# Kernel optimization log

Hardware: AMD Instinct MI355X
Metric: run time of the kernel (lower is better)

The kernel has to match this reference:

```python
import jax, jax.numpy as jnp
import numpy as np

E = 800000
NUM_RADIAL = 6
HIDDEN = 128
OUT = 128
NUM_NODES = 50000


def setup_inputs() -> dict:
    key = jax.random.key(0)
    ks = jax.random.split(key, 12)
    x = jax.random.normal(ks[0], (E, HIDDEN), dtype=jnp.float32)
    rbf = jax.random.uniform(ks[1], (E, NUM_RADIAL), dtype=jnp.float32)
    i = jax.random.randint(ks[2], (E,), 0, NUM_NODES, dtype=jnp.int64)
    s = 1.0 / np.sqrt(HIDDEN)
    W_rbf = jax.random.normal(ks[3], (HIDDEN, NUM_RADIAL), dtype=jnp.float32) / np.sqrt(NUM_RADIAL)
    W1 = jax.random.normal(ks[4], (HIDDEN, HIDDEN), dtype=jnp.float32) * s
    b1 = jnp.zeros((HIDDEN,), dtype=jnp.float32)
    W2 = jax.random.normal(ks[5], (HIDDEN, HIDDEN), dtype=jnp.float32) * s
    b2 = jnp.zeros((HIDDEN,), dtype=jnp.float32)
    W3 = jax.random.normal(ks[6], (HIDDEN, HIDDEN), dtype=jnp.float32) * s
    b3 = jnp.zeros((HIDDEN,), dtype=jnp.float32)
    W_out = jax.random.normal(ks[7], (OUT, HIDDEN), dtype=jnp.float32) * s
    return {"x": x, "rbf": rbf, "i": i, "num_nodes": NUM_NODES,
            "W_rbf": W_rbf, "W1": W1, "b1": b1, "W2": W2, "b2": b2,
            "W3": W3, "b3": b3, "W_out": W_out}


def reference(x, rbf, i, num_nodes, W_rbf, W1, b1, W2, b2, W3, b3, W_out):
    # edge-wise: lin_rbf(rbf) * x, then scatter-add to nodes
    m = (rbf @ W_rbf.T) * x                      # [E, H]
    h = jax.ops.segment_sum(m, i, num_segments=num_nodes)  # [N, H]
    # MLP stack with swish activation
    h = jax.nn.silu(h @ W1.T + b1)
    h = jax.nn.silu(h @ W2.T + b2)
    h = jax.nn.silu(h @ W3.T + b3)
    return h @ W_out.T                           # [N, OUT]
```

## Files before the change

### kernel.cpp

```cpp
#include <hip/hip_runtime.h>
#include <hip/hip_bf16.h>

#define H 128
#define NR 6
#define MT 128
#define HS 136

typedef __attribute__((ext_vector_type(8))) short short8_t;
typedef __attribute__((ext_vector_type(4))) float f32x4;

__device__ __forceinline__ float silu_f(float v) {
    return v / (1.0f + __expf(-v));
}

__device__ __forceinline__ unsigned short bf16_rne(float f) {
    unsigned u = __float_as_uint(f);
    u += 0x7FFF + ((u >> 16) & 1);
    return (unsigned short)(u >> 16);
}
__device__ __forceinline__ float bf16_to_f(unsigned short s) {
    return __uint_as_float(((unsigned)s) << 16);
}

__global__ __launch_bounds__(256) void hist_k(const int* __restrict__ idx,
                                              int* __restrict__ counts, int E) {
    int i = blockIdx.x * 256 + threadIdx.x;
    if (i < E) atomicAdd(&counts[idx[i]], 1);
}

__global__ __launch_bounds__(1024) void scan_k(const int* __restrict__ counts,
                                               int* __restrict__ offsets, int N) {
    __shared__ int wsum[16];
    __shared__ int runv;
    const int tid = threadIdx.x, lane = tid & 63, wv = tid >> 6;
    if (tid == 0) runv = 0;
    __syncthreads();
    for (int base = 0; base < N; base += 1024) {
        const int j = base + tid;
        const int v_in = (j < N) ? counts[j] : 0;
        int v = v_in;
        #pragma unroll
        for (int d = 1; d < 64; d <<= 1) {
            int u = __shfl_up(v, d);
            if (lane >= d) v += u;
        }
        if (lane == 63) wsum[wv] = v;
        __syncthreads();
        if (tid < 16) {
            int s = wsum[tid];
            #pragma unroll
            for (int d = 1; d < 16; d <<= 1) {
                int u = __shfl_up(s, d);
                if (tid >= d) s += u;
            }
            wsum[tid] = s;
        }
        __syncthreads();
        const int wexcl = (wv == 0) ? 0 : wsum[wv - 1];
        const int r0 = runv;
        if (j < N) offsets[j] = r0 + wexcl + (v - v_in);
        const int tot = wsum[15];
        __syncthreads();
        if (tid == 0) runv = r0 + tot;
        __syncthreads();
    }
    if (tid == 0) offsets[N] = runv;
}

__global__ __launch_bounds__(256) void fill_k(const int* __restrict__ idx,
                                              const int* __restrict__ offsets,
                                              int* __restrict__ cursor,
                                              int* __restrict__ elist, int E) {
    int i = blockIdx.x * 256 + threadIdx.x;
    if (i < E) {
        int node = idx[i];
        int pos = atomicAdd(&cursor[node], 1);
        elist[offsets[node] + pos] = i;
    }
}

__global__ __launch_bounds__(256) void gather_k(
    const float* __restrict__ x, const float* __restrict__ rbf,
    const float* __restrict__ W_rbf,
    const int* __restrict__ offsets, const int* __restrict__ elist,
    float* __restrict__ h, int N)
{
    const int t = threadIdx.x;
    const int lane = t & 63;
    const int node = blockIdx.x * 4 + (t >> 6);
    if (node >= N) return;

    const float4* wp = (const float4*)(W_rbf + lane * 12);
    const float4 wa = wp[0], wb = wp[1], wc = wp[2];
    const float wr0[NR] = {wa.x, wa.y, wa.z, wa.w, wb.x, wb.y};
    const float wr1[NR] = {wb.z, wb.w, wc.x, wc.y, wc.z, wc.w};

    const int beg = offsets[node], end = offsets[node + 1];
    float ax = 0.f, ay = 0.f;

    for (int base = beg; base < end; base += 64) {
        const int cnt = min(64, end - base);
        const int e_lane = (lane < cnt) ? elist[base + lane] : 0;
        int p = 0;
        for (; p + 4 <= cnt; p += 4) {
            int ev[4];
            float2 xv[4];
            float2 rv[4][3];
            #pragma unroll
            for (int q = 0; q < 4; ++q) ev[q] = __shfl(e_lane, p + q);
            #pragma unroll
            for (int q = 0; q < 4; ++q) {
                const size_t e = (size_t)ev[q];
                xv[q] = *(const float2*)(x + e * H + lane * 2);
                const float2* rp = (const float2*)(rbf + e * NR);
                rv[q][0] = rp[0]; rv[q][1] = rp[1]; rv[q][2] = rp[2];
            }
            #pragma unroll
            for (int q = 0; q < 4; ++q) {
                const float rr[NR] = {rv[q][0].x, rv[q][0].y, rv[q][1].x,
                                      rv[q][1].y, rv[q][2].x, rv[q][2].y};
                float m0 = 0.f, m1 = 0.f;
                #pragma unroll
                for (int j = 0; j < NR; ++j) { m0 += rr[j] * wr0[j]; m1 += rr[j] * wr1[j]; }
                ax += m0 * xv[q].x;
                ay += m1 * xv[q].y;
            }
        }
        for (; p < cnt; ++p) {
            const size_t e = (size_t)__shfl(e_lane, p);
            const float2 xv0 = *(const float2*)(x + e * H + lane * 2);
            const float2* rp = (const float2*)(rbf + e * NR);
            const float2 ra = rp[0], rb2 = rp[1], rc2 = rp[2];
            const float rr[NR] = {ra.x, ra.y, rb2.x, rb2.y, rc2.x, rc2.y};
            float m0 = 0.f, m1 = 0.f;
            #pragma unroll
            for (int j = 0; j < NR; ++j) { m0 += rr[j] * wr0[j]; m1 += rr[j] * wr1[j]; }
            ax += m0 * xv0.x;
            ay += m1 * xv0.y;
        }
    }
    *(float2*)(h + (size_t)node * H + lane * 2) = make_float2(ax, ay);
}


__device__ __forceinline__ void stage_w_lds(const float* __restrict__ Wg,
        unsigned short* w_hi, unsigned short* w_lo, int t)
{
    for (int i = t * 4; i < H * H; i += 2048) {
        const float4 v = *(const float4*)(Wg + i);
        const int c = i >> 7, k = i & 127;
        ushort4 hi4, lo4;
        hi4.x = bf16_rne(v.x); lo4.x = bf16_rne(v.x - bf16_to_f(hi4.x));
        hi4.y = bf16_rne(v.y); lo4.y = bf16_rne(v.y - bf16_to_f(hi4.y));
        hi4.z = bf16_rne(v.z); lo4.z = bf16_rne(v.z - bf16_to_f(hi4.z));
        hi4.w = bf16_rne(v.w); lo4.w = bf16_rne(v.w - bf16_to_f(hi4.w));
        *(ushort4*)&w_hi[c * HS + k] = hi4;
        *(ushort4*)&w_lo[c * HS + k] = lo4;
    }
}

__device__ __forceinline__ void compute_gemm(
    const unsigned short* h_hi, const unsigned short* h_lo,
    const unsigned short* w_hi, const unsigned short* w_lo,
    const float* bl, int wv, int lr, int quad, f32x4 (&acc)[8])
{
    short8_t a_hi[4], a_lo[4];
    const int row = wv * 16 + lr;
    #pragma unroll
    for (int kb = 0; kb < 4; ++kb) {
        const int off = row * HS + kb * 32 + quad * 8;
        a_hi[kb] = *(const short8_t*)&h_hi[off];
        a_lo[kb] = *(const short8_t*)&h_lo[off];
    }
    #pragma unroll
    for (int ct = 0; ct < 8; ct += 2) {
        const int c0 = ct * 16 + lr, c1 = (ct + 1) * 16 + lr;
        const float bb0 = bl[c0], bb1 = bl[c1];
        f32x4 A0 = {bb0, bb0, bb0, bb0}, A1 = {bb1, bb1, bb1, bb1};
        short8_t b0h[4], b0l[4], b1h[4], b1l[4];
        #pragma unroll
        for (int kb = 0; kb < 4; ++kb) {
            const int o0 = c0 * HS + kb * 32 + quad * 8;
            const int o1 = c1 * HS + kb * 32 + quad * 8;
            b0h[kb] = *(const short8_t*)&w_hi[o0];
            b0l[kb] = *(const short8_t*)&w_lo[o0];
            b1h[kb] = *(const short8_t*)&w_hi[o1];
            b1l[kb] = *(const short8_t*)&w_lo[o1];
        }
        #pragma unroll
        for (int kb = 0; kb < 4; ++kb) {
            A0 = __builtin_amdgcn_mfma_f32_16x16x32_bf16(a_hi[kb], b0h[kb], A0, 0, 0, 0);
            A1 = __builtin_amdgcn_mfma_f32_16x16x32_bf16(a_hi[kb], b1h[kb], A1, 0, 0, 0);
            A0 = __builtin_amdgcn_mfma_f32_16x16x32_bf16(a_hi[kb], b0l[kb], A0, 0, 0, 0);
            A1 = __builtin_amdgcn_mfma_f32_16x16x32_bf16(a_hi[kb], b1l[kb], A1, 0, 0, 0);
            A0 = __builtin_amdgcn_mfma_f32_16x16x32_bf16(a_lo[kb], b0h[kb], A0, 0, 0, 0);
            A1 = __builtin_amdgcn_mfma_f32_16x16x32_bf16(a_lo[kb], b1h[kb], A1, 0, 0, 0);
        }
        acc[ct] = A0;
        acc[ct + 1] = A1;
    }
}

__device__ __forceinline__ void epilogue_silu(
    unsigned short* h_hi, unsigned short* h_lo,
    f32x4 (&acc)[8], int wv, int lr, int quad)
{
    #pragma unroll
    for (int ct = 0; ct < 8; ++ct)
        #pragma unroll
        for (int r = 0; r < 4; ++r) {
            const int row = wv * 16 + quad * 4 + r;
            const int col = ct * 16 + lr;
            const float v = silu_f(acc[ct][r]);
            const unsigned short hi = bf16_rne(v);
            h_hi[row * HS + col] = hi;
            h_lo[row * HS + col] = bf16_rne(v - bf16_to_f(hi));
        }
}

__global__ __launch_bounds__(512, 2) void mlp_mfma(
    const float* __restrict__ hg,
    const float* __restrict__ W1, const float* __restrict__ b1,
    const float* __restrict__ W2, const float* __restrict__ b2,
    const float* __restrict__ W3, const float* __restrict__ b3,
    const float* __restrict__ Wo,
    float* __restrict__ out, int N)
{
    __shared__ unsigned short h_hi[H * HS], h_lo[H * HS];
    __shared__ unsigned short w_hi[H * HS], w_lo[H * HS];
    __shared__ float bl[H];

    const int t = threadIdx.x;
    const int lane = t & 63;
    const int wv = t >> 6;
    const int lr = lane & 15;
    const int quad = lane >> 4;
    const int row0 = blockIdx.x * MT;

    for (int i = t * 4; i < MT * H; i += 2048) {
        const int r = i >> 7, k = i & 127;
        const int row = row0 + r;
        const float4 v = (row < N) ? *(const float4*)(hg + (size_t)row * H + k)
                                   : make_float4(0.f, 0.f, 0.f, 0.f);
        ushort4 hi4, lo4;
        hi4.x = bf16_rne(v.x); lo4.x = bf16_rne(v.x - bf16_to_f(hi4.x));
        hi4.y = bf16_rne(v.y); lo4.y = bf16_rne(v.y - bf16_to_f(hi4.y));
        hi4.z = bf16_rne(v.z); lo4.z = bf16_rne(v.z - bf16_to_f(hi4.z));
        hi4.w = bf16_rne(v.w); lo4.w = bf16_rne(v.w - bf16_to_f(hi4.w));
        *(ushort4*)&h_hi[r * HS + k] = hi4;
        *(ushort4*)&h_lo[r * HS + k] = lo4;
    }
    stage_w_lds(W1, w_hi, w_lo, t);
    if (t < H) bl[t] = b1[t];
    __syncthreads();

    f32x4 acc[8];

    compute_gemm(h_hi, h_lo, w_hi, w_lo, bl, wv, lr, quad, acc);
    __syncthreads();
    epilogue_silu(h_hi, h_lo, acc, wv, lr, quad);
    stage_w_lds(W2, w_hi, w_lo, t);
    if (t < H) bl[t] = b2[t];
    __syncthreads();

    compute_gemm(h_hi, h_lo, w_hi, w_lo, bl, wv, lr, quad, acc);
    __syncthreads();
    epilogue_silu(h_hi, h_lo, acc, wv, lr, quad);
    stage_w_lds(W3, w_hi, w_lo, t);
    if (t < H) bl[t] = b3[t];
    __syncthreads();

    compute_gemm(h_hi, h_lo, w_hi, w_lo, bl, wv, lr, quad, acc);
    __syncthreads();
    epilogue_silu(h_hi, h_lo, acc, wv, lr, quad);
    stage_w_lds(Wo, w_hi, w_lo, t);
    if (t < H) bl[t] = 0.f;
    __syncthreads();

    compute_gemm(h_hi, h_lo, w_hi, w_lo, bl, wv, lr, quad, acc);

    #pragma unroll
    for (int ct = 0; ct < 8; ++ct)
        #pragma unroll
        for (int r = 0; r < 4; ++r) {
            const int row = row0 + wv * 16 + quad * 4 + r;
            if (row < N) out[(size_t)row * H + ct * 16 + lr] = acc[ct][r];
        }
}

static inline size_t align256(size_t v) { return (v + 255) & ~(size_t)255; }

extern "C" void kernel_launch(void* const* d_in, const int* in_sizes, int n_in,
                              void* d_out, int out_size, void* d_ws, size_t ws_size,
                              hipStream_t stream) {
    const float* x     = (const float*)d_in[0];
    const float* rbf   = (const float*)d_in[1];
    const int*   idx   = (const int*)d_in[2];
    const float* W_rbf = (const float*)d_in[4];
    const float* W1    = (const float*)d_in[5];
    const float* b1    = (const float*)d_in[6];
    const float* W2    = (const float*)d_in[7];
    const float* b2    = (const float*)d_in[8];
    const float* W3    = (const float*)d_in[9];
    const float* b3    = (const float*)d_in[10];
    const float* Wo    = (const float*)d_in[11];
    float* out = (float*)d_out;

    const int E = in_sizes[0] / H;
    const int N = out_size / H;

    char* ws = (char*)d_ws;
    size_t off = 0;
    float* h       = (float*)(ws + off); off = align256(off + (size_t)N * H * 4);
    int*   counts  = (int*)(ws + off);   off = align256(off + (size_t)N * 4);
    int*   cursor  = (int*)(ws + off);   off = align256(off + (size_t)N * 4);
    int*   offsets = (int*)(ws + off);   off = align256(off + (size_t)(N + 1) * 4);
    int*   elist   = (int*)(ws + off);   off = align256(off + (size_t)E * 4);

    hipMemsetAsync(counts, 0, (char*)offsets - (char*)counts, stream);

    hist_k<<<(E + 255) / 256, 256, 0, stream>>>(idx, counts, E);
    scan_k<<<1, 1024, 0, stream>>>(counts, offsets, N);
    fill_k<<<(E + 255) / 256, 256, 0, stream>>>(idx, offsets, cursor, elist, E);
    gather_k<<<(N + 3) / 4, 256, 0, stream>>>(x, rbf, W_rbf, offsets, elist, h, N);
    mlp_mfma<<<(N + MT - 1) / MT, 512, 0, stream>>>(h, W1, b1, W2, b2, W3, b3, Wo, out, N);
}
```

Before: 797.6 us.

## Fuse edge gather into MLP kernel and pre-split weights into bf16 hi/lo

Removes the separate gather kernel and its global h buffer. The gather now runs inside the MLP kernel and writes the bf16 hi/lo split straight into shared memory, with each wave handling 16 nodes and half-waves taking alternate edges using float4 loads. Weight hi/lo splitting moves to a small pre-kernel so each MLP block only copies ready-made bf16 data into shared memory. The cost is that the irregular gather now runs inside a large-LDS, low-occupancy block (only ~391 blocks), which can reduce the memory-level parallelism available for the random x reads.

```diff
diff --git a/kernel.cpp b/kernel.cpp
--- a/kernel.cpp
+++ b/kernel.cpp
@@ -1,5 +1,4 @@
 #include <hip/hip_runtime.h>
-#include <hip/hip_bf16.h>
 
 #define H 128
 #define NR 6
@@ -79,83 +78,38 @@
     }
 }
 
-__global__ __launch_bounds__(256) void gather_k(
-    const float* __restrict__ x, const float* __restrict__ rbf,
-    const float* __restrict__ W_rbf,
-    const int* __restrict__ offsets, const int* __restrict__ elist,
-    float* __restrict__ h, int N)
-{
-    const int t = threadIdx.x;
-    const int lane = t & 63;
-    const int node = blockIdx.x * 4 + (t >> 6);
-    if (node >= N) return;
-
-    const float4* wp = (const float4*)(W_rbf + lane * 12);
-    const float4 wa = wp[0], wb = wp[1], wc = wp[2];
-    const float wr0[NR] = {wa.x, wa.y, wa.z, wa.w, wb.x, wb.y};
-    const float wr1[NR] = {wb.z, wb.w, wc.x, wc.y, wc.z, wc.w};
-
-    const int beg = offsets[node], end = offsets[node + 1];
-    float ax = 0.f, ay = 0.f;
-
-    for (int base = beg; base < end; base += 64) {
-        const int cnt = min(64, end - base);
-        const int e_lane = (lane < cnt) ? elist[base + lane] : 0;
-        int p = 0;
-        for (; p + 4 <= cnt; p += 4) {
-            int ev[4];
-            float2 xv[4];
-            float2 rv[4][3];
-            #pragma unroll
-            for (int q = 0; q < 4; ++q) ev[q] = __shfl(e_lane, p + q);
-            #pragma unroll
-            for (int q = 0; q < 4; ++q) {
-                const size_t e = (size_t)ev[q];
-                xv[q] = *(const float2*)(x + e * H + lane * 2);
-                const float2* rp = (const float2*)(rbf + e * NR);
-                rv[q][0] = rp[0]; rv[q][1] = rp[1]; rv[q][2] = rp[2];
-            }
-            #pragma unroll
-            for (int q = 0; q < 4; ++q) {
-                const float rr[NR] = {rv[q][0].x, rv[q][0].y, rv[q][1].x,
-                                      rv[q][1].y, rv[q][2].x, rv[q][2].y};
-                float m0 = 0.f, m1 = 0.f;
-                #pragma unroll
-                for (int j = 0; j < NR; ++j) { m0 += rr[j] * wr0[j]; m1 += rr[j] * wr1[j]; }
-                ax += m0 * xv[q].x;
-                ay += m1 * xv[q].y;
-            }
-        }
-        for (; p < cnt; ++p) {
-            const size_t e = (size_t)__shfl(e_lane, p);
-            const float2 xv0 = *(const float2*)(x + e * H + lane * 2);
-            const float2* rp = (const float2*)(rbf + e * NR);
-            const float2 ra = rp[0], rb2 = rp[1], rc2 = rp[2];
-            const float rr[NR] = {ra.x, ra.y, rb2.x, rb2.y, rc2.x, rc2.y};
-            float m0 = 0.f, m1 = 0.f;
-            #pragma unroll
-            for (int j = 0; j < NR; ++j) { m0 += rr[j] * wr0[j]; m1 += rr[j] * wr1[j]; }
-            ax += m0 * xv0.x;
-            ay += m1 * xv0.y;
-        }
-    }
-    *(float2*)(h + (size_t)node * H + lane * 2) = make_float2(ax, ay);
-}
-
-
-__device__ __forceinline__ void stage_w_lds(const float* __restrict__ Wg,
+__global__ __launch_bounds__(256) void wsplit_k(
+    const float* __restrict__ W1, const float* __restrict__ W2,
+    const float* __restrict__ W3, const float* __restrict__ Wo,
+    unsigned short* __restrict__ dst)
+{
+    const float* W = (blockIdx.y == 0) ? W1 : (blockIdx.y == 1) ? W2
+                   : (blockIdx.y == 2) ? W3 : Wo;
+    unsigned short* hi = dst + (size_t)blockIdx.y * 2 * H * H;
+    unsigned short* lo = hi + H * H;
+    const int i = (blockIdx.x * 256 + threadIdx.x) * 4;
+    if (i < H * H) {
+        const float4 v = *(const float4*)(W + i);
+        ushort4 h4, l4;
+        h4.x = bf16_rne(v.x); l4.x = bf16_rne(v.x - bf16_to_f(h4.x));
+        h4.y = bf16_rne(v.y); l4.y = bf16_rne(v.y - bf16_to_f(h4.y));
+        h4.z = bf16_rne(v.z); l4.z = bf16_rne(v.z - bf16_to_f(h4.z));
+        h4.w = bf16_rne(v.w); l4.w = bf16_rne(v.w - bf16_to_f(h4.w));
+        *(ushort4*)&hi[i] = h4;
+        *(ushort4*)&lo[i] = l4;
+    }
+}
+
+
+__device__ __forceinline__ void stage_w_pre(const unsigned short* __restrict__ g,
         unsigned short* w_hi, unsigned short* w_lo, int t)
 {
-    for (int i = t * 4; i < H * H; i += 2048) {
-        const float4 v = *(const float4*)(Wg + i);
+    const unsigned short* hi_g = g;
+    const unsigned short* lo_g = g + H * H;
+    for (int i = t * 8; i < H * H; i += 4096) {
         const int c = i >> 7, k = i & 127;
-        ushort4 hi4, lo4;
-        hi4.x = bf16_rne(v.x); lo4.x = bf16_rne(v.x - bf16_to_f(hi4.x));
-        hi4.y = bf16_rne(v.y); lo4.y = bf16_rne(v.y - bf16_to_f(hi4.y));
-        hi4.z = bf16_rne(v.z); lo4.z = bf16_rne(v.z - bf16_to_f(hi4.z));
-        hi4.w = bf16_rne(v.w); lo4.w = bf16_rne(v.w - bf16_to_f(hi4.w));
-        *(ushort4*)&w_hi[c * HS + k] = hi4;
-        *(ushort4*)&w_lo[c * HS + k] = lo4;
+        *(short8_t*)&w_hi[c * HS + k] = *(const short8_t*)&hi_g[i];
+        *(short8_t*)&w_lo[c * HS + k] = *(const short8_t*)&lo_g[i];
     }
 }
 
@@ -218,12 +172,13 @@
         }
 }
 
-__global__ __launch_bounds__(512, 2) void mlp_mfma(
-    const float* __restrict__ hg,
-    const float* __restrict__ W1, const float* __restrict__ b1,
-    const float* __restrict__ W2, const float* __restrict__ b2,
-    const float* __restrict__ W3, const float* __restrict__ b3,
-    const float* __restrict__ Wo,
+__global__ __launch_bounds__(512, 2) void fused_mlp(
+    const float* __restrict__ x, const float* __restrict__ rbf,
+    const float* __restrict__ W_rbf,
+    const int* __restrict__ offsets, const int* __restrict__ elist,
+    const unsigned short* __restrict__ wsp,
+    const float* __restrict__ b1, const float* __restrict__ b2,
+    const float* __restrict__ b3,
     float* __restrict__ out, int N)
 {
     __shared__ unsigned short h_hi[H * HS], h_lo[H * HS];
@@ -235,22 +190,83 @@
     const int wv = t >> 6;
     const int lr = lane & 15;
     const int quad = lane >> 4;
+    const int sub = lane >> 5;
+    const int l32 = lane & 31;
     const int row0 = blockIdx.x * MT;
 
-    for (int i = t * 4; i < MT * H; i += 2048) {
-        const int r = i >> 7, k = i & 127;
-        const int row = row0 + r;
-        const float4 v = (row < N) ? *(const float4*)(hg + (size_t)row * H + k)
-                                   : make_float4(0.f, 0.f, 0.f, 0.f);
-        ushort4 hi4, lo4;
-        hi4.x = bf16_rne(v.x); lo4.x = bf16_rne(v.x - bf16_to_f(hi4.x));
-        hi4.y = bf16_rne(v.y); lo4.y = bf16_rne(v.y - bf16_to_f(hi4.y));
-        hi4.z = bf16_rne(v.z); lo4.z = bf16_rne(v.z - bf16_to_f(hi4.z));
-        hi4.w = bf16_rne(v.w); lo4.w = bf16_rne(v.w - bf16_to_f(hi4.w));
-        *(ushort4*)&h_hi[r * HS + k] = hi4;
-        *(ushort4*)&h_lo[r * HS + k] = lo4;
-    }
-    stage_w_lds(W1, w_hi, w_lo, t);
+    const float4* wp = (const float4*)(W_rbf + l32 * 24);
+    const float4 w0 = wp[0], w1 = wp[1], w2 = wp[2], w3 = wp[3],
+                 w4 = wp[4], w5 = wp[5];
+    const float wr[4][NR] = {
+        {w0.x, w0.y, w0.z, w0.w, w1.x, w1.y},
+        {w1.z, w1.w, w2.x, w2.y, w2.z, w2.w},
+        {w3.x, w3.y, w3.z, w3.w, w4.x, w4.y},
+        {w4.z, w4.w, w5.x, w5.y, w5.z, w5.w}};
+
+    for (int i = 0; i < 16; ++i) {
+        const int node = row0 + wv * 16 + i;
+        float4 ga = make_float4(0.f, 0.f, 0.f, 0.f);
+        if (node < N) {
+            const int beg = offsets[node], end = offsets[node + 1];
+            for (int base = beg; base < end; base += 64) {
+                const int cnt = min(64, end - base);
+                const int e_lane = (lane < cnt) ? elist[base + lane] : 0;
+                for (int p = 0; p < cnt; p += 8) {
+                    int ev[4];
+                    bool val[4];
+                    float4 xv[4];
+                    float2 rv[4][3];
+                    #pragma unroll
+                    for (int q = 0; q < 4; ++q) {
+                        const int slot = p + 2 * q + sub;
+                        val[q] = slot < cnt;
+                        ev[q] = __shfl(e_lane, val[q] ? slot : cnt - 1);
+                    }
+                    #pragma unroll
+                    for (int q = 0; q < 4; ++q) {
+                        const size_t e = (size_t)ev[q];
+                        xv[q] = *(const float4*)(x + e * H + l32 * 4);
+                        const float2* rp = (const float2*)(rbf + e * NR);
+                        rv[q][0] = rp[0]; rv[q][1] = rp[1]; rv[q][2] = rp[2];
+                    }
+                    #pragma unroll
+                    for (int q = 0; q < 4; ++q) {
+                        if (!val[q]) continue;
+                        const float rr[NR] = {rv[q][0].x, rv[q][0].y, rv[q][1].x,
+                                              rv[q][1].y, rv[q][2].x, rv[q][2].y};
+                        float s0 = 0.f, s1 = 0.f, s2 = 0.f, s3 = 0.f;
+                        #pragma unroll
+                        for (int j = 0; j < NR; ++j) {
+                            s0 += rr[j] * wr[0][j];
+                            s1 += rr[j] * wr[1][j];
+                            s2 += rr[j] * wr[2][j];
+                            s3 += rr[j] * wr[3][j];
+                        }
+                        ga.x += s0 * xv[q].x;
+                        ga.y += s1 * xv[q].y;
+                        ga.z += s2 * xv[q].z;
+                        ga.w += s3 * xv[q].w;
+                    }
+                }
+            }
+            ga.x += __shfl_xor(ga.x, 32);
+            ga.y += __shfl_xor(ga.y, 32);
+            ga.z += __shfl_xor(ga.z, 32);
+            ga.w += __shfl_xor(ga.w, 32);
+        }
+        if (sub == 0) {
+            ushort4 h4, l4;
+            h4.x = bf16_rne(ga.x); l4.x = bf16_rne(ga.x - bf16_to_f(h4.x));
+            h4.y = bf16_rne(ga.y); l4.y = bf16_rne(ga.y - bf16_to_f(h4.y));
+            h4.z = bf16_rne(ga.z); l4.z = bf16_rne(ga.z - bf16_to_f(h4.z));
+            h4.w = bf16_rne(ga.w); l4.w = bf16_rne(ga.w - bf16_to_f(h4.w));
+            const int off = (wv * 16 + i) * HS + l32 * 4;
+            *(ushort4*)&h_hi[off] = h4;
+            *(ushort4*)&h_lo[off] = l4;
+        }
+    }
+
+    stage_w_pre(wsp, w_hi, w_lo, t);
     if (t < H) bl[t] = b1[t];
     __syncthreads();
 
@@ -259,21 +275,21 @@
     compute_gemm(h_hi, h_lo, w_hi, w_lo, bl, wv, lr, quad, acc);
     __syncthreads();
     epilogue_silu(h_hi, h_lo, acc, wv, lr, quad);
-    stage_w_lds(W2, w_hi, w_lo, t);
+    stage_w_pre(wsp + 32768, w_hi, w_lo, t);
     if (t < H) bl[t] = b2[t];
     __syncthreads();
 
     compute_gemm(h_hi, h_lo, w_hi, w_lo, bl, wv, lr, quad, acc);
     __syncthreads();
     epilogue_silu(h_hi, h_lo, acc, wv, lr, quad);
-    stage_w_lds(W3, w_hi, w_lo, t);
+    stage_w_pre(wsp + 65536, w_hi, w_lo, t);
     if (t < H) bl[t] = b3[t];
     __syncthreads();
 
     compute_gemm(h_hi, h_lo, w_hi, w_lo, bl, wv, lr, quad, acc);
     __syncthreads();
     epilogue_silu(h_hi, h_lo, acc, wv, lr, quad);
-    stage_w_lds(Wo, w_hi, w_lo, t);
+    stage_w_pre(wsp + 98304, w_hi, w_lo, t);
     if (t < H) bl[t] = 0.f;
     __syncthreads();
 
@@ -311,17 +327,19 @@
 
     char* ws = (char*)d_ws;
     size_t off = 0;
-    float* h       = (float*)(ws + off); off = align256(off + (size_t)N * H * 4);
-    int*   counts  = (int*)(ws + off);   off = align256(off + (size_t)N * 4);
-    int*   cursor  = (int*)(ws + off);   off = align256(off + (size_t)N * 4);
-    int*   offsets = (int*)(ws + off);   off = align256(off + (size_t)(N + 1) * 4);
-    int*   elist   = (int*)(ws + off);   off = align256(off + (size_t)E * 4);
+    unsigned short* wsp = (unsigned short*)(ws + off);
+    off = align256(off + (size_t)4 * 2 * H * H * sizeof(unsigned short));
+    int* counts  = (int*)(ws + off);   off = align256(off + (size_t)N * 4);
+    int* cursor  = (int*)(ws + off);   off = align256(off + (size_t)N * 4);
+    int* offsets = (int*)(ws + off);   off = align256(off + (size_t)(N + 1) * 4);
+    int* elist   = (int*)(ws + off);   off = align256(off + (size_t)E * 4);
 
     hipMemsetAsync(counts, 0, (char*)offsets - (char*)counts, stream);
 
+    wsplit_k<<<dim3(16, 4), 256, 0, stream>>>(W1, W2, W3, Wo, wsp);
     hist_k<<<(E + 255) / 256, 256, 0, stream>>>(idx, counts, E);
     scan_k<<<1, 1024, 0, stream>>>(counts, offsets, N);
     fill_k<<<(E + 255) / 256, 256, 0, stream>>>(idx, offsets, cursor, elist, E);
-    gather_k<<<(N + 3) / 4, 256, 0, stream>>>(x, rbf, W_rbf, offsets, elist, h, N);
-    mlp_mfma<<<(N + MT - 1) / MT, 512, 0, stream>>>(h, W1, b1, W2, b2, W3, b3, Wo, out, N);
-}
+    fused_mlp<<<(N + MT - 1) / MT, 512, 0, stream>>>(
+        x, rbf, W_rbf, offsets, elist, wsp, b1, b2, b3, out, N);
+}
```

Result: faster. 774.4 us (-2.9%).
